# Performance work log

Measured on AMD Instinct MI355X. Metric: run time of the kernel, lower is better.

The kernel has to match this reference:

```python
import jax, jax.numpy as jnp
from jax import lax
import numpy as np

# Interactions from init: (is_inclusion, label_A, label_C)
INTERACTIONS = [(True, 1, 2), (False, 1, 3)]
# 26-connectivity, min_thick=1 -> 3x3x3 ones structuring element (OIDHW layout)
KERNEL = jnp.ones((1, 1, 3, 3, 3), jnp.float32)
NUM_CLASSES = 4


def _dilate(mask):
    # binary dilation: all-ones conv then threshold >= 1 (matches conv3d + where)
    c = lax.conv_general_dilated(
        mask, KERNEL, window_strides=(1, 1, 1), padding='SAME',
        dimension_numbers=('NCDHW', 'OIDHW', 'NCDHW'))
    return (c >= 1.0).astype(jnp.float32)


def _critical_voxels(P):
    # P: (b,1,D,H,W) float discrete segmentation map
    crit = None
    for is_inclusion, label_A, label_C in INTERACTIONS:
        mask_A = (P == label_A).astype(jnp.float32)
        mask_C = (P == label_C).astype(jnp.float32)
        if is_inclusion:
            # C := not (C or A)
            mask_C = 1.0 - jnp.maximum(mask_C, mask_A)
        violating = (_dilate(mask_C) * mask_A + _dilate(mask_A) * mask_C >= 1.0).astype(jnp.float32)
        crit = violating if crit is None else jnp.maximum(crit, violating)
    return crit


def setup_inputs() -> dict:
    key = jax.random.key(0)
    kx, ky = jax.random.split(key)
    x = jax.random.normal(kx, (2, NUM_CLASSES, 128, 128, 128), dtype=jnp.float32)
    y = jax.random.randint(ky, (2, 1, 128, 128, 128), 0, NUM_CLASSES, dtype=jnp.int64)
    return {"x": x, "y": y}


def reference(x, y):
    # discrete prediction map (argmax of softmax == argmax of logits)
    P = jnp.argmax(jax.nn.softmax(x, axis=1), axis=1)[:, None].astype(jnp.float32)  # (b,1,D,H,W)
    crit = _critical_voxels(P)  # (b,1,D,H,W)
    # per-voxel cross entropy: -log_softmax(x)[y]
    logp = jax.nn.log_softmax(x, axis=1)
    ce = -jnp.take_along_axis(logp, y.astype(jnp.int32), axis=1)[:, 0]  # (b,D,H,W)
    masked = ce * crit[:, 0]
    return masked.sum(axis=(1, 2, 3)).mean()
```

## Files before the change

kernel.cpp:

```cpp
#include <hip/hip_runtime.h>

constexpr int Dd = 128, Hh = 128, Ww = 128;
constexpr int NVOX = Dd * Hh * Ww;
constexpr int NB = 2;
constexpr int NC = 4;
constexpr int TOTAL = NB * NVOX;
constexpr int NWORDS = TOTAL / 64;

struct alignas(16) MaskW { unsigned long long m1, m03; };

__global__ __launch_bounds__(256) void argmax_ce_kernel(
    const float* __restrict__ x, const int* __restrict__ y,
    MaskW* __restrict__ Mw, float* __restrict__ ce)
{
    int tid = threadIdx.x;
    int lane = tid & 63;
    int wavebase = blockIdx.x * 1024 + (tid >> 6) * 256;
    int b = wavebase >> 21;
    int vb = wavebase & (NVOX - 1);
    const float* xb = x + (size_t)b * NC * NVOX;

    unsigned long long w1[4], w03[4];
    #pragma unroll
    for (int j = 0; j < 4; ++j) {
        int v = vb + 64 * j + lane;
        int g = wavebase + 64 * j + lane;
        float x0 = xb[v];
        float x1 = xb[v + NVOX];
        float x2 = xb[v + 2 * NVOX];
        float x3 = xb[v + 3 * NVOX];
        int p = 0; float m = x0;
        if (x1 > m) { m = x1; p = 1; }
        if (x2 > m) { m = x2; p = 2; }
        if (x3 > m) { m = x3; p = 3; }
        float s = expf(x0 - m) + expf(x1 - m) + expf(x2 - m) + expf(x3 - m);
        int yy = y[g];
        float xy = (yy == 0) ? x0 : ((yy == 1) ? x1 : ((yy == 2) ? x2 : x3));
        ce[g] = m + logf(s) - xy;
        w1[j]  = __ballot(p == 1);
        w03[j] = __ballot(p == 0 || p == 3);
    }
    if (lane == 0) {
        int wbase = wavebase >> 6;
        #pragma unroll
        for (int j = 0; j < 4; ++j) {
            MaskW mw; mw.m1 = w1[j]; mw.m03 = w03[j];
            Mw[wbase + j] = mw;
        }
    }
}

__global__ __launch_bounds__(256) void crit_sum_kernel(
    const MaskW* __restrict__ Mw, const float* __restrict__ ce,
    float* __restrict__ out)
{
    __shared__ unsigned long long sm1[3][256];
    __shared__ unsigned long long sm03[3][256];
    __shared__ unsigned long long critw[256];
    __shared__ float wsum[4];

    int tid = threadIdx.x;
    int bid = blockIdx.x;
    int d = bid & 127;

    #pragma unroll
    for (int pl = 0; pl < 3; ++pl) {
        int dp = d - 1 + pl;
        unsigned long long a = 0, c = 0;
        if ((unsigned)dp < 128u) {
            MaskW m = Mw[(bid - d + dp) * 256 + tid];
            a = m.m1; c = m.m03;
        }
        sm1[pl][tid] = a;
        sm03[pl][tid] = c;
    }
    __syncthreads();

    int h = tid >> 1, k = tid & 1;
    unsigned long long E1 = 0, E03 = 0;
    #pragma unroll
    for (int pl = 0; pl < 3; ++pl) {
        #pragma unroll
        for (int dy = -1; dy <= 1; ++dy) {
            int hh = h + dy;
            if ((unsigned)hh < 128u) {
                int idx = hh * 2 + k;
                int adj = hh * 2 + (k ^ 1);
                unsigned long long m1 = sm1[pl][idx],  a1 = sm1[pl][adj];
                unsigned long long m3 = sm03[pl][idx], a3 = sm03[pl][adj];
                unsigned long long s1 = m1 | (m1 << 1) | (m1 >> 1);
                unsigned long long s3 = m3 | (m3 << 1) | (m3 >> 1);
                if (k == 0) { s1 |= (a1 & 1ull) << 63; s3 |= (a3 & 1ull) << 63; }
                else        { s1 |= (a1 >> 63);        s3 |= (a3 >> 63); }
                E1  |= s1;
                E03 |= s3;
            }
        }
    }
    unsigned long long C1 = sm1[1][tid], C03 = sm03[1][tid];
    critw[tid] = (C1 & E03) | (C03 & E1);
    __syncthreads();

    const float4* cep = (const float4*)(ce + ((size_t)bid << 14));
    float s = 0.f;
    #pragma unroll
    for (int j = 0; j < 16; ++j) {
        float4 c = cep[j * 256 + tid];
        unsigned long long w = critw[j * 16 + (tid >> 4)];
        int bb = (tid & 15) * 4;
        if ((w >> bb)       & 1ull) s += c.x;
        if ((w >> (bb + 1)) & 1ull) s += c.y;
        if ((w >> (bb + 2)) & 1ull) s += c.z;
        if ((w >> (bb + 3)) & 1ull) s += c.w;
    }
    #pragma unroll
    for (int off = 32; off; off >>= 1) s += __shfl_down(s, off, 64);
    if ((tid & 63) == 0) wsum[tid >> 6] = s;
    __syncthreads();
    if (tid == 0) {
        float t = wsum[0] + wsum[1] + wsum[2] + wsum[3];
        atomicAdd(out, t * 0.5f);
    }
}

extern "C" void kernel_launch(void* const* d_in, const int* in_sizes, int n_in,
                              void* d_out, int out_size, void* d_ws, size_t ws_size,
                              hipStream_t stream) {
    const float* x = (const float*)d_in[0];
    const int*   y = (const int*)d_in[1];
    MaskW* Mw = (MaskW*)d_ws;
    float* ce = (float*)((char*)d_ws + (size_t)NWORDS * 16);
    float* out = (float*)d_out;

    hipMemsetAsync(out, 0, sizeof(float), stream);
    argmax_ce_kernel<<<TOTAL / 1024, 256, 0, stream>>>(x, y, Mw, ce);
    crit_sum_kernel<<<NB * Dd, 256, 0, stream>>>(Mw, ce, out);
}
```

Before: 114.8 us.

## Store CE intermediate as bf16, vectorize loads, fold memset into first kernel

The per-voxel cross-entropy intermediate is now stored as bf16 instead of fp32, which halves its write and read traffic between the two kernels. The first kernel switches to float4/int4 vector loads with four voxels per thread. Mask words are assembled from per-thread nibbles through shared memory instead of wave ballots. The output memset is folded into the first kernel, removing one launch. The cost is rounding each CE term to bf16 before summation, which can introduce small accuracy error in the final sum.

```diff
diff --git a/kernel.cpp b/kernel.cpp
--- a/kernel.cpp
+++ b/kernel.cpp
@@ -9,49 +9,75 @@
 
 struct alignas(16) MaskW { unsigned long long m1, m03; };
 
+__device__ __forceinline__ unsigned short f2bf(float f) {
+    unsigned int u = __float_as_uint(f);
+    return (unsigned short)((u + 0x7FFFu + ((u >> 16) & 1u)) >> 16);
+}
+__device__ __forceinline__ float bf2f_lo(unsigned int u) { return __uint_as_float(u << 16); }
+__device__ __forceinline__ float bf2f_hi(unsigned int u) { return __uint_as_float(u & 0xFFFF0000u); }
+
 __global__ __launch_bounds__(256) void argmax_ce_kernel(
-    const float* __restrict__ x, const int* __restrict__ y,
-    MaskW* __restrict__ Mw, float* __restrict__ ce)
+    const float4* __restrict__ x4, const int4* __restrict__ y4,
+    MaskW* __restrict__ Mw, unsigned short* __restrict__ ce,
+    float* __restrict__ out)
 {
     int tid = threadIdx.x;
-    int lane = tid & 63;
-    int wavebase = blockIdx.x * 1024 + (tid >> 6) * 256;
-    int b = wavebase >> 21;
-    int vb = wavebase & (NVOX - 1);
-    const float* xb = x + (size_t)b * NC * NVOX;
+    if (blockIdx.x == 0 && tid == 0) out[0] = 0.f;
 
-    unsigned long long w1[4], w03[4];
+    int gv = blockIdx.x * 256 + tid;
+    int b  = gv >> 19;
+    int vv = gv & ((NVOX / 4) - 1);
+    const float4* xb = x4 + (size_t)b * (NC * NVOX / 4) + vv;
+    float4 a0 = xb[0];
+    float4 a1 = xb[NVOX / 4];
+    float4 a2 = xb[2 * (NVOX / 4)];
+    float4 a3 = xb[3 * (NVOX / 4)];
+    int4 yi = y4[gv];
+
+    float X0[4] = {a0.x, a0.y, a0.z, a0.w};
+    float X1[4] = {a1.x, a1.y, a1.z, a1.w};
+    float X2[4] = {a2.x, a2.y, a2.z, a2.w};
+    float X3[4] = {a3.x, a3.y, a3.z, a3.w};
+    int   Y[4]  = {yi.x, yi.y, yi.z, yi.w};
+
+    unsigned int nib1 = 0, nib03 = 0;
+    unsigned short cv[4];
     #pragma unroll
-    for (int j = 0; j < 4; ++j) {
-        int v = vb + 64 * j + lane;
-        int g = wavebase + 64 * j + lane;
-        float x0 = xb[v];
-        float x1 = xb[v + NVOX];
-        float x2 = xb[v + 2 * NVOX];
-        float x3 = xb[v + 3 * NVOX];
+    for (int c = 0; c < 4; ++c) {
+        float x0 = X0[c], x1 = X1[c], x2 = X2[c], x3 = X3[c];
         int p = 0; float m = x0;
         if (x1 > m) { m = x1; p = 1; }
         if (x2 > m) { m = x2; p = 2; }
         if (x3 > m) { m = x3; p = 3; }
         float s = expf(x0 - m) + expf(x1 - m) + expf(x2 - m) + expf(x3 - m);
-        int yy = y[g];
+        int yy = Y[c];
         float xy = (yy == 0) ? x0 : ((yy == 1) ? x1 : ((yy == 2) ? x2 : x3));
-        ce[g] = m + logf(s) - xy;
-        w1[j]  = __ballot(p == 1);
-        w03[j] = __ballot(p == 0 || p == 3);
+        cv[c] = f2bf(m + logf(s) - xy);
+        nib1  |= (unsigned)(p == 1) << c;
+        nib03 |= (unsigned)(p == 0 || p == 3) << c;
     }
-    if (lane == 0) {
-        int wbase = wavebase >> 6;
+    ushort4 cev = {cv[0], cv[1], cv[2], cv[3]};
+    ((ushort4*)ce)[gv] = cev;
+
+    __shared__ unsigned int nibs[256];
+    nibs[tid] = nib1 | (nib03 << 8);
+    __syncthreads();
+    if (tid < 16) {
+        int base = tid * 16;
+        unsigned long long m1 = 0, m03 = 0;
         #pragma unroll
-        for (int j = 0; j < 4; ++j) {
-            MaskW mw; mw.m1 = w1[j]; mw.m03 = w03[j];
-            Mw[wbase + j] = mw;
+        for (int k = 0; k < 16; ++k) {
+            unsigned int nv = nibs[base + k];
+            m1  |= (unsigned long long)(nv & 0xFu) << (4 * k);
+            m03 |= (unsigned long long)((nv >> 8) & 0xFu) << (4 * k);
         }
+        MaskW mw; mw.m1 = m1; mw.m03 = m03;
+        Mw[blockIdx.x * 16 + tid] = mw;
     }
 }
 
 __global__ __launch_bounds__(256) void crit_sum_kernel(
-    const MaskW* __restrict__ Mw, const float* __restrict__ ce,
+    const MaskW* __restrict__ Mw, const unsigned short* __restrict__ ce,
     float* __restrict__ out)
 {
     __shared__ unsigned long long sm1[3][256];
@@ -101,17 +127,22 @@
     critw[tid] = (C1 & E03) | (C03 & E1);
     __syncthreads();
 
-    const float4* cep = (const float4*)(ce + ((size_t)bid << 14));
+    const uint4* cep = (const uint4*)(ce + ((size_t)bid << 14));
     float s = 0.f;
     #pragma unroll
-    for (int j = 0; j < 16; ++j) {
-        float4 c = cep[j * 256 + tid];
-        unsigned long long w = critw[j * 16 + (tid >> 4)];
-        int bb = (tid & 15) * 4;
-        if ((w >> bb)       & 1ull) s += c.x;
-        if ((w >> (bb + 1)) & 1ull) s += c.y;
-        if ((w >> (bb + 2)) & 1ull) s += c.z;
-        if ((w >> (bb + 3)) & 1ull) s += c.w;
+    for (int j = 0; j < 8; ++j) {
+        int idx = j * 256 + tid;
+        uint4 u = cep[idx];
+        unsigned long long w = critw[idx >> 3];
+        int bb = (idx & 7) * 8;
+        if ((w >> bb)       & 1ull) s += bf2f_lo(u.x);
+        if ((w >> (bb + 1)) & 1ull) s += bf2f_hi(u.x);
+        if ((w >> (bb + 2)) & 1ull) s += bf2f_lo(u.y);
+        if ((w >> (bb + 3)) & 1ull) s += bf2f_hi(u.y);
+        if ((w >> (bb + 4)) & 1ull) s += bf2f_lo(u.z);
+        if ((w >> (bb + 5)) & 1ull) s += bf2f_hi(u.z);
+        if ((w >> (bb + 6)) & 1ull) s += bf2f_lo(u.w);
+        if ((w >> (bb + 7)) & 1ull) s += bf2f_hi(u.w);
     }
     #pragma unroll
     for (int off = 32; off; off >>= 1) s += __shfl_down(s, off, 64);
@@ -126,13 +157,12 @@
 extern "C" void kernel_launch(void* const* d_in, const int* in_sizes, int n_in,
                               void* d_out, int out_size, void* d_ws, size_t ws_size,
                               hipStream_t stream) {
-    const float* x = (const float*)d_in[0];
-    const int*   y = (const int*)d_in[1];
+    const float4* x4 = (const float4*)d_in[0];
+    const int4*   y4 = (const int4*)d_in[1];
     MaskW* Mw = (MaskW*)d_ws;
-    float* ce = (float*)((char*)d_ws + (size_t)NWORDS * 16);
+    unsigned short* ce = (unsigned short*)((char*)d_ws + (size_t)NWORDS * 16);
     float* out = (float*)d_out;
 
-    hipMemsetAsync(out, 0, sizeof(float), stream);
-    argmax_ce_kernel<<<TOTAL / 1024, 256, 0, stream>>>(x, y, Mw, ce);
+    argmax_ce_kernel<<<TOTAL / 1024, 256, 0, stream>>>(x4, y4, Mw, ce, out);
     crit_sum_kernel<<<NB * Dd, 256, 0, stream>>>(Mw, ce, out);
 }
```

Result: faster. 107.7 us (-6.2%).
